# Kernel optimization log

Hardware: AMD Instinct MI355X
Metric: run time of the kernel (lower is better)

## Reference

```python
import jax, jax.numpy as jnp
import numpy as np
import math

B, L, DV = 8, 2048, 512
FACTOR = 5
SAMPLE_K = min(FACTOR * int(np.ceil(np.log(L))), L)  # 40
N_TOP = min(FACTOR * int(np.ceil(np.log(L))), L)     # 40


def setup_inputs() -> dict:
    key = jax.random.key(0)
    k1, k2, k3, k4, k5 = jax.random.split(key, 5)
    x = jax.random.normal(k1, (B, L, DV), dtype=jnp.float32)
    Wq = jax.random.normal(k2, (DV, DV), dtype=jnp.float32) * (1.0 / math.sqrt(DV))
    Wk = jax.random.normal(k3, (DV, DV), dtype=jnp.float32) * (1.0 / math.sqrt(DV))
    Wv = jax.random.normal(k4, (DV, DV), dtype=jnp.float32) * (1.0 / math.sqrt(DV))
    index_sample = jax.random.randint(k5, (L, SAMPLE_K), 0, L, dtype=jnp.int32)
    return {"x": x, "Wq": Wq, "Wk": Wk, "Wv": Wv, "index_sample": index_sample}


def reference(x, Wq, Wk, Wv, index_sample):
    # Projections (torch Linear, no bias): y = x @ W.T
    Q = x @ Wq.T  # [B, L, D]
    K = x @ Wk.T  # [B, L, D]
    V = x @ Wv.T  # [B, L, D]
    b, L_Q, D = Q.shape
    L_K = K.shape[1]

    # _prob_QK: sample keys per query, score sparsity measure M
    K_sample = K[:, index_sample, :]                       # [B, L_Q, sample_k, D]
    QK_sample = jnp.einsum('bld,blsd->bls', Q, K_sample)   # [B, L_Q, sample_k]
    M = QK_sample.max(axis=-1) - QK_sample.sum(axis=-1) / L_K  # [B, L_Q]
    _, M_top = jax.lax.top_k(M, N_TOP)                     # [B, n_top]

    Q_reduce = jnp.take_along_axis(Q, M_top[:, :, None], axis=1)  # [B, n_top, D]
    scores = jnp.einsum('bud,bkd->buk', Q_reduce, K)       # [B, n_top, L_K]
    scores = scores * (1.0 / math.sqrt(D))

    # mask_flag=False -> initial context is mean of V broadcast over queries
    attn = jax.nn.softmax(scores, axis=-1)
    context = jnp.broadcast_to(V.mean(axis=1, keepdims=True), (b, L_Q, D))
    upd = attn @ V                                         # [B, n_top, D]
    context = context.at[jnp.arange(b)[:, None], M_top].set(upd)
    return context
```

## Files before the change

### kernel.cpp

```cpp
#include <hip/hip_runtime.h>
#include <hip/hip_bf16.h>
#include <math.h>

#define BATCH 8
#define LSEQ 2048
#define DIM 512
#define SK 40
#define NTOP 40

typedef __attribute__((ext_vector_type(8))) short bf16x8;
typedef __attribute__((ext_vector_type(4))) float f32x4;

__device__ inline void split1(float f, ushort& h, ushort& l) {
    __hip_bfloat16 bh = __float2bfloat16(f);
    float r = f - __bfloat162float(bh);
    __hip_bfloat16 bl = __float2bfloat16(r);
    h = *reinterpret_cast<ushort*>(&bh);
    l = *reinterpret_cast<ushort*>(&bl);
}

__global__ __launch_bounds__(256) void convert_all(
    const float* __restrict__ x,
    const float* __restrict__ w0, const float* __restrict__ w1, const float* __restrict__ w2,
    ushort* __restrict__ xh, ushort* __restrict__ xl,
    ushort* __restrict__ wh, ushort* __restrict__ wl)
{
    const int bx = blockIdx.x;
    const float* src;
    ushort *dh, *dl;
    int i;
    if (bx < 8192) {
        i = (bx * 256 + (int)threadIdx.x) * 4;
        src = x; dh = xh; dl = xl;
    } else {
        const int j = bx - 8192;
        const int z = j >> 8;
        src = (z == 0) ? w0 : (z == 1) ? w1 : w2;
        dh = wh + (size_t)z * DIM * DIM;
        dl = wl + (size_t)z * DIM * DIM;
        i = ((j & 255) * 256 + (int)threadIdx.x) * 4;
    }
    float4 v = *reinterpret_cast<const float4*>(src + i);
    ushort4 h, l;
    split1(v.x, h.x, l.x); split1(v.y, h.y, l.y);
    split1(v.z, h.z, l.z); split1(v.w, h.w, l.w);
    *reinterpret_cast<ushort4*>(dh + i) = h;
    *reinterpret_cast<ushort4*>(dl + i) = l;
}

__device__ inline void load_lds16(const void* g, void* l) {
    __builtin_amdgcn_global_load_lds(
        (const __attribute__((address_space(1))) void*)g,
        (__attribute__((address_space(3))) void*)l, 16, 0, 0);
}

__global__ __launch_bounds__(256) void gemm_mfma(
    const ushort* __restrict__ xh, const ushort* __restrict__ xl,
    const ushort* __restrict__ whAll, const ushort* __restrict__ wlAll,
    float* __restrict__ Q, float* __restrict__ K, float* __restrict__ V)
{
    const ushort* Wh = whAll + (size_t)blockIdx.z * DIM * DIM;
    const ushort* Wl = wlAll + (size_t)blockIdx.z * DIM * DIM;
    float* C = (blockIdx.z == 0) ? Q : (blockIdx.z == 1) ? K : V;

    __shared__ ushort Ah[128 * 32], Al[128 * 32], Bh[128 * 32], Bl[128 * 32];

    const int tid  = threadIdx.x;
    const int lane = tid & 63;
    const int w    = tid >> 6;
    const int row0 = blockIdx.x * 128;
    const int col0 = blockIdx.y * 128;
    const int wr = w >> 1, wc = w & 1;

    const int rA  = w * 16 + (lane >> 2);
    const int sh_ = (lane & 3) ^ ((rA >> 1) & 3);
    const size_t aoff = (size_t)(row0 + rA) * DIM + sh_ * 8;
    const size_t boff = (size_t)(col0 + rA) * DIM + sh_ * 8;

    f32x4 acc[4][4];
    #pragma unroll
    for (int i = 0; i < 4; ++i)
        #pragma unroll
        for (int j = 0; j < 4; ++j)
            acc[i][j] = (f32x4){0.f, 0.f, 0.f, 0.f};

    const int rbA = wr * 64 + (lane & 15);
    const int rbB = wc * 64 + (lane & 15);
    const int kh  = lane >> 4;

    for (int k0 = 0; k0 < DIM; k0 += 32) {
        load_lds16(xh + aoff + k0,            &Ah[w * 512]);
        load_lds16(xh + aoff + 64 * DIM + k0, &Ah[2048 + w * 512]);
        load_lds16(xl + aoff + k0,            &Al[w * 512]);
        load_lds16(xl + aoff + 64 * DIM + k0, &Al[2048 + w * 512]);
        load_lds16(Wh + boff + k0,            &Bh[w * 512]);
        load_lds16(Wh + boff + 64 * DIM + k0, &Bh[2048 + w * 512]);
        load_lds16(Wl + boff + k0,            &Bl[w * 512]);
        load_lds16(Wl + boff + 64 * DIM + k0, &Bl[2048 + w * 512]);
        __syncthreads();

        bf16x8 fah[4], fal[4], fbh[4], fbl[4];
        #pragma unroll
        for (int mf = 0; mf < 4; ++mf) {
            const int r = rbA + mf * 16;
            const int off = r * 32 + (kh ^ ((r >> 1) & 3)) * 8;
            fah[mf] = *reinterpret_cast<const bf16x8*>(&Ah[off]);
            fal[mf] = *reinterpret_cast<const bf16x8*>(&Al[off]);
        }
        #pragma unroll
        for (int nf = 0; nf < 4; ++nf) {
            const int r = rbB + nf * 16;
            const int off = r * 32 + (kh ^ ((r >> 1) & 3)) * 8;
            fbh[nf] = *reinterpret_cast<const bf16x8*>(&Bh[off]);
            fbl[nf] = *reinterpret_cast<const bf16x8*>(&Bl[off]);
        }
        #pragma unroll
        for (int mf = 0; mf < 4; ++mf)
            #pragma unroll
            for (int nf = 0; nf < 4; ++nf) {
                acc[mf][nf] = __builtin_amdgcn_mfma_f32_16x16x32_bf16(fah[mf], fbh[nf], acc[mf][nf], 0, 0, 0);
                acc[mf][nf] = __builtin_amdgcn_mfma_f32_16x16x32_bf16(fal[mf], fbh[nf], acc[mf][nf], 0, 0, 0);
                acc[mf][nf] = __builtin_amdgcn_mfma_f32_16x16x32_bf16(fah[mf], fbl[nf], acc[mf][nf], 0, 0, 0);
            }
        __syncthreads();
    }

    #pragma unroll
    for (int mf = 0; mf < 4; ++mf)
        #pragma unroll
        for (int nf = 0; nf < 4; ++nf) {
            float* cp = C + (size_t)(row0 + wr * 64 + mf * 16 + (lane >> 4) * 4) * DIM
                          + col0 + wc * 64 + nf * 16 + (lane & 15);
            #pragma unroll
            for (int j = 0; j < 4; ++j)
                cp[(size_t)j * DIM] = acc[mf][nf][j];
        }
}

#define BM 64
#define BN 64
#define BKD 32
__global__ __launch_bounds__(256) void gemm_qkv(
    const float* __restrict__ x,
    const float* __restrict__ Wq, const float* __restrict__ Wk, const float* __restrict__ Wv,
    float* __restrict__ Q, float* __restrict__ K, float* __restrict__ V)
{
    const float* W;
    float* C;
    if (blockIdx.z == 0)      { W = Wq; C = Q; }
    else if (blockIdx.z == 1) { W = Wk; C = K; }
    else                      { W = Wv; C = V; }

    __shared__ float As[BKD][BM];
    __shared__ float Bs[BKD][BN];

    const int tid  = threadIdx.x;
    const int row0 = blockIdx.x * BM;
    const int col0 = blockIdx.y * BN;
    const int ty   = tid >> 4;
    const int tx   = tid & 15;
    const int lrow = tid >> 3;
    const int lkq  = tid & 7;

    float acc[4][4] = {};
    for (int k0 = 0; k0 < DIM; k0 += BKD) {
        #pragma unroll
        for (int h = 0; h < 2; ++h) {
            const int arow = lrow + h * 32;
            float4 va = *reinterpret_cast<const float4*>(&x[(size_t)(row0 + arow) * DIM + k0 + lkq * 4]);
            As[lkq * 4 + 0][arow] = va.x; As[lkq * 4 + 1][arow] = va.y;
            As[lkq * 4 + 2][arow] = va.z; As[lkq * 4 + 3][arow] = va.w;
            float4 vb = *reinterpret_cast<const float4*>(&W[(size_t)(col0 + arow) * DIM + k0 + lkq * 4]);
            Bs[lkq * 4 + 0][arow] = vb.x; Bs[lkq * 4 + 1][arow] = vb.y;
            Bs[lkq * 4 + 2][arow] = vb.z; Bs[lkq * 4 + 3][arow] = vb.w;
        }
        __syncthreads();
        #pragma unroll
        for (int kk = 0; kk < BKD; ++kk) {
            float4 a4 = *reinterpret_cast<const float4*>(&As[kk][ty * 4]);
            float4 b4 = *reinterpret_cast<const float4*>(&Bs[kk][tx * 4]);
            float af[4] = {a4.x, a4.y, a4.z, a4.w};
            float bf[4] = {b4.x, b4.y, b4.z, b4.w};
            #pragma unroll
            for (int i = 0; i < 4; ++i)
                #pragma unroll
                for (int j = 0; j < 4; ++j)
                    acc[i][j] += af[i] * bf[j];
        }
        __syncthreads();
    }
    #pragma unroll
    for (int i = 0; i < 4; ++i) {
        float4 o = make_float4(acc[i][0], acc[i][1], acc[i][2], acc[i][3]);
        *reinterpret_cast<float4*>(&C[(size_t)(row0 + ty * 4 + i) * DIM + col0 + tx * 4]) = o;
    }
}

__global__ __launch_bounds__(512) void m_and_vp(
    const float* __restrict__ Q, const float* __restrict__ K,
    const float* __restrict__ V, const int* __restrict__ smp,
    float* __restrict__ M, float* __restrict__ P)
{
    const int bid = blockIdx.x;
    if (bid < 2048) {
        const int wv   = threadIdx.x >> 6;
        const int lane = threadIdx.x & 63;
        const int b    = bid & 7;
        const int l    = (bid >> 3) * 8 + wv;

        const float* qr = Q + ((size_t)b * LSEQ + l) * DIM;
        float4 q0 = *reinterpret_cast<const float4*>(&qr[lane * 8]);
        float4 q1 = *reinterpret_cast<const float4*>(&qr[lane * 8 + 4]);

        const int* sp = smp + l * SK;
        const float* Kb = K + (size_t)b * LSEQ * DIM;

        float mx = -1e30f, sm = 0.0f;
        for (int s = 0; s < SK; s += 8) {
            int4 i0 = *reinterpret_cast<const int4*>(sp + s);
            int4 i1 = *reinterpret_cast<const int4*>(sp + s + 4);
            const int id[8] = {i0.x, i0.y, i0.z, i0.w, i1.x, i1.y, i1.z, i1.w};
            float p[8];
            #pragma unroll
            for (int j = 0; j < 8; ++j) {
                const float* r = Kb + (size_t)id[j] * DIM + lane * 8;
                float4 u0 = *reinterpret_cast<const float4*>(r);
                float4 u1 = *reinterpret_cast<const float4*>(r + 4);
                p[j] = q0.x*u0.x + q0.y*u0.y + q0.z*u0.z + q0.w*u0.w
                     + q1.x*u1.x + q1.y*u1.y + q1.z*u1.z + q1.w*u1.w;
            }
            #pragma unroll
            for (int o = 32; o; o >>= 1) {
                #pragma unroll
                for (int j = 0; j < 8; ++j) p[j] += __shfl_xor(p[j], o, 64);
            }
            #pragma unroll
            for (int j = 0; j < 8; ++j) { mx = fmaxf(mx, p[j]); sm += p[j]; }
        }
        if (lane == 0) M[(size_t)b * LSEQ + l] = mx - sm * (1.0f / LSEQ);
    } else {
        const int j = bid - 2048;
        const int b = j & 7, c = j >> 3;
        const int d = threadIdx.x;
        const float* vp = V + ((size_t)b * LSEQ + c * 128) * DIM + d;
        float s = 0.0f;
        for (int r = 0; r < 128; ++r) s += vp[(size_t)r * DIM];
        P[(size_t)(b * 16 + c) * DIM + d] = s;
    }
}

__global__ __launch_bounds__(512) void topk_vr(
    const float* __restrict__ M, const float* __restrict__ P,
    int* __restrict__ topidx, float* __restrict__ vmean)
{
    __shared__ float vals[LSEQ];
    __shared__ float wvv[8];
    __shared__ int   wii[8];

    if (blockIdx.x < 8) {
        const int b = blockIdx.x;
        const int tid  = threadIdx.x;
        const int lane = tid & 63;
        const int wave = tid >> 6;

        #pragma unroll
        for (int q = 0; q < 4; ++q) vals[tid + q * 512] = M[b * LSEQ + tid + q * 512];
        __syncthreads();

        for (int t = 0; t < NTOP; ++t) {
            float bv = -1e30f;
            int   bi = 0x7fffffff;
            #pragma unroll
            for (int q = 0; q < 4; ++q) {
                const int ii = tid + q * 512;
                const float v = vals[ii];
                if (v > bv) { bv = v; bi = ii; }
            }
            #pragma unroll
            for (int o = 32; o; o >>= 1) {
                float ov = __shfl_xor(bv, o, 64);
                int   oi = __shfl_xor(bi, o, 64);
                if (ov > bv || (ov == bv && oi < bi)) { bv = ov; bi = oi; }
            }
            if (lane == 0) { wvv[wave] = bv; wii[wave] = bi; }
            __syncthreads();
            if (wave == 0) {
                float fv = (lane < 8) ? wvv[lane] : -1e30f;
                int   fi = (lane < 8) ? wii[lane] : 0x7fffffff;
                #pragma unroll
                for (int o = 4; o; o >>= 1) {
                    float ov = __shfl_xor(fv, o, 64);
                    int   oi = __shfl_xor(fi, o, 64);
                    if (ov > fv || (ov == fv && oi < fi)) { fv = ov; fi = oi; }
                }
                if (lane == 0) {
                    topidx[b * NTOP + t] = fi;
                    vals[fi] = -1e30f;
                }
            }
            __syncthreads();
        }
    } else {
        const int b = blockIdx.x - 8;
        const int d = threadIdx.x;
        float s = 0.0f;
        #pragma unroll
        for (int c = 0; c < 16; ++c) s += P[(size_t)(b * 16 + c) * DIM + d];
        vmean[b * DIM + d] = s * (1.0f / LSEQ);
    }
}

__global__ __launch_bounds__(256) void fill_out(
    const float4* __restrict__ vmean4, float4* __restrict__ out4)
{
    const int f = blockIdx.x * 256 + threadIdx.x;
    const int d4 = f & 127;
    const int b  = f >> 18;
    out4[f] = vmean4[b * 128 + d4];
}

__global__ __launch_bounds__(256) void scores_kernel(
    const float* __restrict__ Q, const float* __restrict__ K,
    const int* __restrict__ topidx, float* __restrict__ S)
{
    const int b  = blockIdx.x & 7;
    const int lc = blockIdx.x >> 3;
    __shared__ float Qs[40 * 132];
    __shared__ float Ks[64 * 132];
    __shared__ int tix[NTOP];
    const int tid = threadIdx.x;
    const int lt  = tid & 31;
    const int ug  = tid >> 5;
    float acc[2][5] = {};

    if (tid < NTOP) tix[tid] = topidx[b * NTOP + tid];
    __syncthreads();

    for (int d0 = 0; d0 < DIM; d0 += 128) {
        for (int j = tid; j < 1280; j += 256) {
            const int u = j >> 5, d4 = j & 31;
            *reinterpret_cast<float4*>(&Qs[u * 132 + d4 * 4]) =
                *reinterpret_cast<const float4*>(&Q[((size_t)b * LSEQ + tix[u]) * DIM + d0 + d4 * 4]);
        }
        for (int j = tid; j < 2048; j += 256) {
            const int l = j >> 5, d4 = j & 31;
            *reinterpret_cast<float4*>(&Ks[l * 132 + d4 * 4]) =
                *reinterpret_cast<const float4*>(&K[((size_t)b * LSEQ + lc * 64 + l) * DIM + d0 + d4 * 4]);
        }
        __syncthreads();
        for (int d4 = 0; d4 < 32; ++d4) {
            float4 ka = *reinterpret_cast<const float4*>(&Ks[lt * 132 + d4 * 4]);
            float4 kb = *reinterpret_cast<const float4*>(&Ks[(lt + 32) * 132 + d4 * 4]);
            #pragma unroll
            for (int i = 0; i < 5; ++i) {
                float4 q = *reinterpret_cast<const float4*>(&Qs[(ug + i * 8) * 132 + d4 * 4]);
                acc[0][i] += q.x * ka.x + q.y * ka.y + q.z * ka.z + q.w * ka.w;
                acc[1][i] += q.x * kb.x + q.y * kb.y + q.z * kb.z + q.w * kb.w;
            }
        }
        __syncthreads();
    }
    const float scale = 0.044194173824159216f;
    #pragma unroll
    for (int i = 0; i < 5; ++i) {
        const int u = ug + i * 8;
        S[((size_t)(b * NTOP + u)) * LSEQ + lc * 64 + lt]      = acc[0][i] * scale;
        S[((size_t)(b * NTOP + u)) * LSEQ + lc * 64 + lt + 32] = acc[1][i] * scale;
    }
}

__global__ __launch_bounds__(256) void softmax_kernel(
    const float* __restrict__ S, float* __restrict__ Pt)
{
    const int row = blockIdx.x;
    const int b = row / NTOP, u = row % NTOP;
    __shared__ float red[4];
    const int tid  = threadIdx.x;
    const int lane = tid & 63;
    const int wave = tid >> 6;
    const float* sr = S + (size_t)row * LSEQ;

    float v[8];
    float mx = -1e30f;
    #pragma unroll
    for (int j = 0; j < 8; ++j) { v[j] = sr[tid + j * 256]; mx = fmaxf(mx, v[j]); }
    #pragma unroll
    for (int o = 32; o; o >>= 1) mx = fmaxf(mx, __shfl_xor(mx, o, 64));
    if (lane == 0) red[wave] = mx;
    __syncthreads();
    mx = fmaxf(fmaxf(red[0], red[1]), fmaxf(red[2], red[3]));
    __syncthreads();

    float s = 0.0f;
    #pragma unroll
    for (int j = 0; j < 8; ++j) { v[j] = __expf(v[j] - mx); s += v[j]; }
    #pragma unroll
    for (int o = 32; o; o >>= 1) s += __shfl_xor(s, o, 64);
    if (lane == 0) red[wave] = s;
    __syncthreads();
    const float rec = 1.0f / (red[0] + red[1] + red[2] + red[3]);

    #pragma unroll
    for (int j = 0; j < 8; ++j)
        Pt[((size_t)b * LSEQ + tid + j * 256) * NTOP + u] = v[j] * rec;
}

__global__ __launch_bounds__(512) void pv_partial(
    const float* __restrict__ Pt, const float* __restrict__ V, float* __restrict__ Ppart)
{
    const int b  = blockIdx.x & 7;
    const int lc = blockIdx.x >> 3;
    const int d  = threadIdx.x;
    float part[NTOP] = {};
    for (int l = 0; l < 128; ++l) {
        const float v = V[((size_t)b * LSEQ + lc * 128 + l) * DIM + d];
        const float* ps = Pt + ((size_t)b * LSEQ + lc * 128 + l) * NTOP;
        #pragma unroll
        for (int u = 0; u < NTOP; ++u) part[u] = fmaf(ps[u], v, part[u]);
    }
    #pragma unroll
    for (int u = 0; u < NTOP; ++u)
        Ppart[(((size_t)(b * 16 + lc)) * NTOP + u) * DIM + d] = part[u];
}

__global__ __launch_bounds__(512) void pv_reduce(
    const float* __restrict__ Ppart, const int* __restrict__ topidx, float* __restrict__ out)
{
    const int row = blockIdx.x;
    const int b = row / NTOP, u = row % NTOP;
    const int d = threadIdx.x;
    float s = 0.0f;
    #pragma unroll
    for (int lc = 0; lc < 16; ++lc)
        s += Ppart[(((size_t)(b * 16 + lc)) * NTOP + u) * DIM + d];
    out[((size_t)b * LSEQ + topidx[row]) * DIM + d] = s;
}

__global__ __launch_bounds__(256) void att_kernel(
    const float* __restrict__ Q, const float* __restrict__ K, const float* __restrict__ V,
    const int* __restrict__ topidx, float* __restrict__ out)
{
    const int b = blockIdx.x / NTOP;
    const int u = blockIdx.x % NTOP;
    const int l0 = topidx[b * NTOP + u];

    __shared__ float p[LSEQ];
    __shared__ float redm[4];
    __shared__ float reds[4];

    const int tid  = threadIdx.x;
    const int lane = tid & 63;
    const int wave = tid >> 6;

    const float* qr = Q + ((size_t)b * LSEQ + l0) * DIM;
    float4 q0 = *reinterpret_cast<const float4*>(&qr[lane * 8]);
    float4 q1 = *reinterpret_cast<const float4*>(&qr[lane * 8 + 4]);
    const float scale = 0.044194173824159216f;

    for (int it = 0; it < 512; ++it) {
        const int l = wave * 512 + it;
        const float* kr = K + ((size_t)b * LSEQ + l) * DIM;
        float4 k0 = *reinterpret_cast<const float4*>(&kr[lane * 8]);
        float4 k1 = *reinterpret_cast<const float4*>(&kr[lane * 8 + 4]);
        float d = q0.x * k0.x + q0.y * k0.y + q0.z * k0.z + q0.w * k0.w
                + q1.x * k1.x + q1.y * k1.y + q1.z * k1.z + q1.w * k1.w;
        #pragma unroll
        for (int o = 32; o; o >>= 1) d += __shfl_xor(d, o, 64);
        if (lane == 0) p[l] = d * scale;
    }
    __syncthreads();

    float mx = -1e30f;
    for (int i = tid; i < LSEQ; i += 256) mx = fmaxf(mx, p[i]);
    #pragma unroll
    for (int o = 32; o; o >>= 1) mx = fmaxf(mx, __shfl_xor(mx, o, 64));
    if (lane == 0) redm[wave] = mx;
    __syncthreads();
    mx = fmaxf(fmaxf(redm[0], redm[1]), fmaxf(redm[2], redm[3]));

    float s = 0.0f;
    for (int i = tid; i < LSEQ; i += 256) {
        float e = __expf(p[i] - mx);
        s += e;
        p[i] = e;
    }
    #pragma unroll
    for (int o = 32; o; o >>= 1) s += __shfl_xor(s, o, 64);
    if (lane == 0) reds[wave] = s;
    __syncthreads();
    const float rec = 1.0f / (reds[0] + reds[1] + reds[2] + reds[3]);

    float s0 = 0.0f, s1 = 0.0f;
    const float* vp = V + (size_t)b * LSEQ * DIM;
    for (int l = 0; l < LSEQ; ++l) {
        const float w = p[l];
        s0 += w * vp[(size_t)l * DIM + tid];
        s1 += w * vp[(size_t)l * DIM + tid + 256];
    }
    float* orow = out + ((size_t)b * LSEQ + l0) * DIM;
    orow[tid]       = s0 * rec;
    orow[tid + 256] = s1 * rec;
}

extern "C" void kernel_launch(void* const* d_in, const int* in_sizes, int n_in,
                              void* d_out, int out_size, void* d_ws, size_t ws_size,
                              hipStream_t stream)
{
    const float* x   = (const float*)d_in[0];
    const float* Wq  = (const float*)d_in[1];
    const float* Wk  = (const float*)d_in[2];
    const float* Wv  = (const float*)d_in[3];
    const int*   smp = (const int*)d_in[4];
    float* out = (float*)d_out;

    const size_t NQKV = (size_t)BATCH * LSEQ * DIM;
    float* ws = (float*)d_ws;

    float* Q     = ws;
    float* K     = Q + NQKV;
    float* V     = K + NQKV;
    float* Mb    = V + NQKV;
    float* vmP   = Mb + BATCH * LSEQ;
    float* vmean = vmP + BATCH * 16 * DIM;
    float* S     = vmean + BATCH * DIM;
    float* Pt    = S + (size_t)BATCH * NTOP * LSEQ;
    float* Qsel  = Pt + (size_t)BATCH * NTOP * LSEQ;
    float* Ppart = Qsel + (size_t)BATCH * NTOP * DIM;
    int*   topidx = (int*)(Ppart + (size_t)BATCH * 16 * NTOP * DIM);
    ushort* xh = (ushort*)(topidx + BATCH * NTOP);
    ushort* xl = xh + NQKV;
    ushort* wh = xl + NQKV;
    ushort* wl = wh + (size_t)3 * DIM * DIM;
    const size_t need_fast = (size_t)((char*)(wl + (size_t)3 * DIM * DIM) - (char*)d_ws);
    const size_t need_mid  = (size_t)((char*)(topidx + BATCH * NTOP) - (char*)d_ws);

    const bool fast = ws_size >= need_fast;
    const bool mid  = ws_size >= need_mid;

    if (mid) {
        if (fast) {
            convert_all<<<8960, 256, 0, stream>>>(x, Wq, Wk, Wv, xh, xl, wh, wl);
            gemm_mfma<<<dim3(BATCH * LSEQ / 128, DIM / 128, 3), 256, 0, stream>>>(
                xh, xl, wh, wl, Q, K, V);
        } else {
            gemm_qkv<<<dim3(BATCH * LSEQ / BM, DIM / BN, 3), 256, 0, stream>>>(
                x, Wq, Wk, Wv, Q, K, V);
        }
        m_and_vp<<<2176, 512, 0, stream>>>(Q, K, V, smp, Mb, vmP);
        topk_vr<<<16, 512, 0, stream>>>(Mb, vmP, topidx, vmean);
        fill_out<<<(BATCH * LSEQ * DIM / 4) / 256, 256, 0, stream>>>(
            (const float4*)vmean, (float4*)out);
        scores_kernel<<<256, 256, 0, stream>>>(Q, K, topidx, S);
        softmax_kernel<<<BATCH * NTOP, 256, 0, stream>>>(S, Pt);
        pv_partial<<<128, 512, 0, stream>>>(Pt, V, Ppart);
        pv_reduce<<<BATCH * NTOP, 512, 0, stream>>>(Ppart, topidx, out);
    } else {
        float* Qf = ws;
        float* Kf = Qf + NQKV;
        float* Vf = Kf + NQKV;
        float* Mf = Vf + NQKV;
        int*   ti = (int*)(Mf + (size_t)BATCH * LSEQ);
        float* Pf = (float*)(ti + BATCH * NTOP);
        float* vm = Pf + (size_t)BATCH * 16 * DIM;

        gemm_qkv<<<dim3(BATCH * LSEQ / BM, DIM / BN, 3), 256, 0, stream>>>(
            x, Wq, Wk, Wv, Qf, Kf, Vf);
        m_and_vp<<<2176, 512, 0, stream>>>(Qf, Kf, Vf, smp, Mf, Pf);
        topk_vr<<<16, 512, 0, stream>>>(Mf, Pf, ti, vm);
        fill_out<<<(BATCH * LSEQ * DIM / 4) / 256, 256, 0, stream>>>(
            (const float4*)vm, (float4*)out);
        att_kernel<<<BATCH * NTOP, 256, 0, stream>>>(Qf, Kf, Vf, ti, out);
    }
}
```

Baseline: 306.6 us.

## Score sparsity with fp16 K copy, refine top-k candidates in fp32

The QKV GEMM epilogue now also writes an fp16 copy of K, and the sampled-key sparsity scores read this half-width copy to cut gather traffic. Top-k is replaced by a radix-style threshold search that keeps 48-128 candidates, recomputes their scores exactly in fp32, and selects the final 40 within one wave. The PV partial kernel is also unrolled over four rows with float4 loads of the probabilities. This adds extra fp16 stores in the GEMM and a serial threshold search, and it risks picking different indices if fp16 error pushes a true top-40 query outside the candidate window.

```diff
diff --git a/kernel.cpp b/kernel.cpp
--- a/kernel.cpp
+++ b/kernel.cpp
@@ -1,5 +1,6 @@
 #include <hip/hip_runtime.h>
 #include <hip/hip_bf16.h>
+#include <hip/hip_fp16.h>
 #include <math.h>
 
 #define BATCH 8
@@ -57,11 +58,13 @@
 __global__ __launch_bounds__(256) void gemm_mfma(
     const ushort* __restrict__ xh, const ushort* __restrict__ xl,
     const ushort* __restrict__ whAll, const ushort* __restrict__ wlAll,
-    float* __restrict__ Q, float* __restrict__ K, float* __restrict__ V)
+    float* __restrict__ Q, float* __restrict__ K, float* __restrict__ V,
+    ushort* __restrict__ Khalf)
 {
     const ushort* Wh = whAll + (size_t)blockIdx.z * DIM * DIM;
     const ushort* Wl = wlAll + (size_t)blockIdx.z * DIM * DIM;
     float* C = (blockIdx.z == 0) ? Q : (blockIdx.z == 1) ? K : V;
+    const bool wk = (Khalf != nullptr) && (blockIdx.z == 1);
 
     __shared__ ushort Ah[128 * 32], Al[128 * 32], Bh[128 * 32], Bl[128 * 32];
 
@@ -129,11 +132,17 @@
     for (int mf = 0; mf < 4; ++mf)
         #pragma unroll
         for (int nf = 0; nf < 4; ++nf) {
-            float* cp = C + (size_t)(row0 + wr * 64 + mf * 16 + (lane >> 4) * 4) * DIM
-                          + col0 + wc * 64 + nf * 16 + (lane & 15);
-            #pragma unroll
-            for (int j = 0; j < 4; ++j)
+            const size_t rbase = (size_t)(row0 + wr * 64 + mf * 16 + (lane >> 4) * 4);
+            const int    cidx  = col0 + wc * 64 + nf * 16 + (lane & 15);
+            float* cp = C + rbase * DIM + cidx;
+            #pragma unroll
+            for (int j = 0; j < 4; ++j) {
                 cp[(size_t)j * DIM] = acc[mf][nf][j];
+                if (wk) {
+                    __half h = __float2half(acc[mf][nf][j]);
+                    Khalf[(rbase + j) * DIM + cidx] = *reinterpret_cast<ushort*>(&h);
+                }
+            }
         }
 }
 
@@ -198,6 +207,7 @@
 
 __global__ __launch_bounds__(512) void m_and_vp(
     const float* __restrict__ Q, const float* __restrict__ K,
+    const ushort* __restrict__ Khalf,
     const float* __restrict__ V, const int* __restrict__ smp,
     float* __restrict__ M, float* __restrict__ P)
 {
@@ -211,31 +221,58 @@
         const float* qr = Q + ((size_t)b * LSEQ + l) * DIM;
         float4 q0 = *reinterpret_cast<const float4*>(&qr[lane * 8]);
         float4 q1 = *reinterpret_cast<const float4*>(&qr[lane * 8 + 4]);
+        const float qf[8] = {q0.x, q0.y, q0.z, q0.w, q1.x, q1.y, q1.z, q1.w};
 
         const int* sp = smp + l * SK;
-        const float* Kb = K + (size_t)b * LSEQ * DIM;
-
         float mx = -1e30f, sm = 0.0f;
-        for (int s = 0; s < SK; s += 8) {
-            int4 i0 = *reinterpret_cast<const int4*>(sp + s);
-            int4 i1 = *reinterpret_cast<const int4*>(sp + s + 4);
-            const int id[8] = {i0.x, i0.y, i0.z, i0.w, i1.x, i1.y, i1.z, i1.w};
-            float p[8];
-            #pragma unroll
-            for (int j = 0; j < 8; ++j) {
-                const float* r = Kb + (size_t)id[j] * DIM + lane * 8;
-                float4 u0 = *reinterpret_cast<const float4*>(r);
-                float4 u1 = *reinterpret_cast<const float4*>(r + 4);
-                p[j] = q0.x*u0.x + q0.y*u0.y + q0.z*u0.z + q0.w*u0.w
-                     + q1.x*u1.x + q1.y*u1.y + q1.z*u1.z + q1.w*u1.w;
-            }
-            #pragma unroll
-            for (int o = 32; o; o >>= 1) {
+
+        if (Khalf) {
+            const ushort* Kb = Khalf + (size_t)b * LSEQ * DIM;
+            for (int s = 0; s < SK; s += 8) {
+                int4 i0 = *reinterpret_cast<const int4*>(sp + s);
+                int4 i1 = *reinterpret_cast<const int4*>(sp + s + 4);
+                const int id[8] = {i0.x, i0.y, i0.z, i0.w, i1.x, i1.y, i1.z, i1.w};
+                float p[8];
                 #pragma unroll
-                for (int j = 0; j < 8; ++j) p[j] += __shfl_xor(p[j], o, 64);
-            }
-            #pragma unroll
-            for (int j = 0; j < 8; ++j) { mx = fmaxf(mx, p[j]); sm += p[j]; }
+                for (int j = 0; j < 8; ++j) {
+                    float4 hv = *reinterpret_cast<const float4*>(Kb + (size_t)id[j] * DIM + lane * 8);
+                    const __half* h = reinterpret_cast<const __half*>(&hv);
+                    float d = 0.0f;
+                    #pragma unroll
+                    for (int e = 0; e < 8; ++e) d = fmaf(qf[e], __half2float(h[e]), d);
+                    p[j] = d;
+                }
+                #pragma unroll
+                for (int o = 32; o; o >>= 1) {
+                    #pragma unroll
+                    for (int j = 0; j < 8; ++j) p[j] += __shfl_xor(p[j], o, 64);
+                }
+                #pragma unroll
+                for (int j = 0; j < 8; ++j) { mx = fmaxf(mx, p[j]); sm += p[j]; }
+            }
+        } else {
+            const float* Kb = K + (size_t)b * LSEQ * DIM;
+            for (int s = 0; s < SK; s += 8) {
+                int4 i0 = *reinterpret_cast<const int4*>(sp + s);
+                int4 i1 = *reinterpret_cast<const int4*>(sp + s + 4);
+                const int id[8] = {i0.x, i0.y, i0.z, i0.w, i1.x, i1.y, i1.z, i1.w};
+                float p[8];
+                #pragma unroll
+                for (int j = 0; j < 8; ++j) {
+                    const float* r = Kb + (size_t)id[j] * DIM + lane * 8;
+                    float4 u0 = *reinterpret_cast<const float4*>(r);
+                    float4 u1 = *reinterpret_cast<const float4*>(r + 4);
+                    p[j] = q0.x*u0.x + q0.y*u0.y + q0.z*u0.z + q0.w*u0.w
+                         + q1.x*u1.x + q1.y*u1.y + q1.z*u1.z + q1.w*u1.w;
+                }
+                #pragma unroll
+                for (int o = 32; o; o >>= 1) {
+                    #pragma unroll
+                    for (int j = 0; j < 8; ++j) p[j] += __shfl_xor(p[j], o, 64);
+                }
+                #pragma unroll
+                for (int j = 0; j < 8; ++j) { mx = fmaxf(mx, p[j]); sm += p[j]; }
+            }
         }
         if (lane == 0) M[(size_t)b * LSEQ + l] = mx - sm * (1.0f / LSEQ);
     } else {
@@ -249,64 +286,139 @@
     }
 }
 
-__global__ __launch_bounds__(512) void topk_vr(
-    const float* __restrict__ M, const float* __restrict__ P,
+__device__ inline unsigned int fkey(float f) {
+    unsigned int b = __float_as_uint(f);
+    return b ^ ((b & 0x80000000u) ? 0xFFFFFFFFu : 0x80000000u);
+}
+
+__global__ __launch_bounds__(1024) void topk_refine(
+    const float* __restrict__ M, const float* __restrict__ Q,
+    const float* __restrict__ K, const int* __restrict__ smp,
+    const float* __restrict__ P,
     int* __restrict__ topidx, float* __restrict__ vmean)
 {
-    __shared__ float vals[LSEQ];
-    __shared__ float wvv[8];
-    __shared__ int   wii[8];
-
-    if (blockIdx.x < 8) {
-        const int b = blockIdx.x;
-        const int tid  = threadIdx.x;
-        const int lane = tid & 63;
-        const int wave = tid >> 6;
-
-        #pragma unroll
-        for (int q = 0; q < 4; ++q) vals[tid + q * 512] = M[b * LSEQ + tid + q * 512];
-        __syncthreads();
-
+    if (blockIdx.x >= 8) {
+        const int b = blockIdx.x - 8;
+        const int d = threadIdx.x;
+        if (d < DIM) {
+            float s = 0.0f;
+            #pragma unroll
+            for (int c = 0; c < 16; ++c) s += P[(size_t)(b * 16 + c) * DIM + d];
+            vmean[b * DIM + d] = s * (1.0f / LSEQ);
+        }
+        return;
+    }
+
+    const int b    = blockIdx.x;
+    const int tid  = threadIdx.x;
+    const int lane = tid & 63;
+    const int wave = tid >> 6;
+
+    __shared__ int   cand[1024];
+    __shared__ float Mex[1024];
+    __shared__ int   scnt[16];
+    __shared__ int   sh_tot;
+    __shared__ int   sh_ccnt;
+
+    const unsigned int k0 = fkey(M[(size_t)b * LSEQ + tid]);
+    const unsigned int k1 = fkey(M[(size_t)b * LSEQ + tid + 1024]);
+    Mex[tid] = -1e30f;
+    if (tid == 0) sh_ccnt = 0;
+    __syncthreads();
+
+    unsigned int lo = 0u, hi = 0xFFFFFFFFu, T = 0u, Tbest = 0u;
+    int found = 0;
+    for (int it = 0; it < 32; ++it) {
+        unsigned int mid = lo + ((hi - lo) >> 1);
+        int c = (k0 > mid ? 1 : 0) + (k1 > mid ? 1 : 0);
+        #pragma unroll
+        for (int o = 32; o; o >>= 1) c += __shfl_xor(c, o, 64);
+        if (lane == 0) scnt[wave] = c;
+        __syncthreads();
+        if (tid == 0) {
+            int t2 = 0;
+            #pragma unroll
+            for (int ww = 0; ww < 16; ++ww) t2 += scnt[ww];
+            sh_tot = t2;
+        }
+        __syncthreads();
+        const int tot = sh_tot;
+        __syncthreads();
+        if (tot >= 48 && tot <= 128) { T = mid; found = 1; break; }
+        if (tot >= 48 && mid > Tbest) Tbest = mid;
+        if (tot > 128) { if (mid == 0xFFFFFFFFu) break; lo = mid + 1; }
+        else           { if (mid == 0u) break; hi = mid - 1; }
+        if (lo > hi) break;
+    }
+    if (!found) T = Tbest;
+
+    if (k0 > T) { int p = atomicAdd(&sh_ccnt, 1); if (p < 1024) cand[p] = tid; }
+    if (k1 > T) { int p = atomicAdd(&sh_ccnt, 1); if (p < 1024) cand[p] = tid + 1024; }
+    __syncthreads();
+    const int n = min(sh_ccnt, 1024);
+
+    for (int j = wave; j < n; j += 16) {
+        const int l = cand[j];
+        const float* qr = Q + ((size_t)b * LSEQ + l) * DIM;
+        float4 q0 = *reinterpret_cast<const float4*>(&qr[lane * 8]);
+        float4 q1 = *reinterpret_cast<const float4*>(&qr[lane * 8 + 4]);
+        const int* sp = smp + l * SK;
+        const float* Kb = K + (size_t)b * LSEQ * DIM;
+        float mx = -1e30f, sm = 0.0f;
+        for (int s = 0; s < SK; s += 8) {
+            int4 i0 = *reinterpret_cast<const int4*>(sp + s);
+            int4 i1 = *reinterpret_cast<const int4*>(sp + s + 4);
+            const int id[8] = {i0.x, i0.y, i0.z, i0.w, i1.x, i1.y, i1.z, i1.w};
+            float p[8];
+            #pragma unroll
+            for (int jj = 0; jj < 8; ++jj) {
+                const float* r = Kb + (size_t)id[jj] * DIM + lane * 8;
+                float4 u0 = *reinterpret_cast<const float4*>(r);
+                float4 u1 = *reinterpret_cast<const float4*>(r + 4);
+                p[jj] = q0.x*u0.x + q0.y*u0.y + q0.z*u0.z + q0.w*u0.w
+                      + q1.x*u1.x + q1.y*u1.y + q1.z*u1.z + q1.w*u1.w;
+            }
+            #pragma unroll
+            for (int o = 32; o; o >>= 1) {
+                #pragma unroll
+                for (int jj = 0; jj < 8; ++jj) p[jj] += __shfl_xor(p[jj], o, 64);
+            }
+            #pragma unroll
+            for (int jj = 0; jj < 8; ++jj) { mx = fmaxf(mx, p[jj]); sm += p[jj]; }
+        }
+        if (lane == 0) Mex[j] = mx - sm * (1.0f / LSEQ);
+    }
+    __syncthreads();
+
+    if (wave == 0) {
+        float lv[16];
+        int   cl[16];
+        #pragma unroll
+        for (int kk = 0; kk < 16; ++kk) {
+            const int j = lane + kk * 64;
+            lv[kk] = Mex[j];
+            cl[kk] = cand[j];
+        }
         for (int t = 0; t < NTOP; ++t) {
-            float bv = -1e30f;
-            int   bi = 0x7fffffff;
-            #pragma unroll
-            for (int q = 0; q < 4; ++q) {
-                const int ii = tid + q * 512;
-                const float v = vals[ii];
-                if (v > bv) { bv = v; bi = ii; }
-            }
+            float bv = -1e30f; int bl = 0x7fffffff; int bk = -1;
+            #pragma unroll
+            for (int kk = 0; kk < 16; ++kk) {
+                if (lv[kk] > bv || (lv[kk] == bv && cl[kk] < bl)) {
+                    bv = lv[kk]; bl = cl[kk]; bk = kk;
+                }
+            }
+            int blane = lane;
             #pragma unroll
             for (int o = 32; o; o >>= 1) {
                 float ov = __shfl_xor(bv, o, 64);
-                int   oi = __shfl_xor(bi, o, 64);
-                if (ov > bv || (ov == bv && oi < bi)) { bv = ov; bi = oi; }
-            }
-            if (lane == 0) { wvv[wave] = bv; wii[wave] = bi; }
-            __syncthreads();
-            if (wave == 0) {
-                float fv = (lane < 8) ? wvv[lane] : -1e30f;
-                int   fi = (lane < 8) ? wii[lane] : 0x7fffffff;
-                #pragma unroll
-                for (int o = 4; o; o >>= 1) {
-                    float ov = __shfl_xor(fv, o, 64);
-                    int   oi = __shfl_xor(fi, o, 64);
-                    if (ov > fv || (ov == fv && oi < fi)) { fv = ov; fi = oi; }
-                }
-                if (lane == 0) {
-                    topidx[b * NTOP + t] = fi;
-                    vals[fi] = -1e30f;
-                }
-            }
-            __syncthreads();
-        }
-    } else {
-        const int b = blockIdx.x - 8;
-        const int d = threadIdx.x;
-        float s = 0.0f;
-        #pragma unroll
-        for (int c = 0; c < 16; ++c) s += P[(size_t)(b * 16 + c) * DIM + d];
-        vmean[b * DIM + d] = s * (1.0f / LSEQ);
+                int   ol = __shfl_xor(bl, o, 64);
+                int   oln = __shfl_xor(blane, o, 64);
+                int   obk = __shfl_xor(bk, o, 64);
+                if (ov > bv || (ov == bv && ol < bl)) { bv = ov; bl = ol; blane = oln; bk = obk; }
+            }
+            if (lane == 0) topidx[b * NTOP + t] = bl;
+            if (lane == blane) lv[bk] = -1e30f;
+        }
     }
 }
 
@@ -412,11 +524,24 @@
     const int lc = blockIdx.x >> 3;
     const int d  = threadIdx.x;
     float part[NTOP] = {};
-    for (int l = 0; l < 128; ++l) {
-        const float v = V[((size_t)b * LSEQ + lc * 128 + l) * DIM + d];
-        const float* ps = Pt + ((size_t)b * LSEQ + lc * 128 + l) * NTOP;
-        #pragma unroll
-        for (int u = 0; u < NTOP; ++u) part[u] = fmaf(ps[u], v, part[u]);
+    for (int lg = 0; lg < 32; ++lg) {
+        const int l = lc * 128 + lg * 4;
+        const float v0 = V[((size_t)b * LSEQ + l + 0) * DIM + d];
+        const float v1 = V[((size_t)b * LSEQ + l + 1) * DIM + d];
+        const float v2 = V[((size_t)b * LSEQ + l + 2) * DIM + d];
+        const float v3 = V[((size_t)b * LSEQ + l + 3) * DIM + d];
+        const float4* p0 = reinterpret_cast<const float4*>(Pt + ((size_t)b * LSEQ + l + 0) * NTOP);
+        const float4* p1 = reinterpret_cast<const float4*>(Pt + ((size_t)b * LSEQ + l + 1) * NTOP);
+        const float4* p2 = reinterpret_cast<const float4*>(Pt + ((size_t)b * LSEQ + l + 2) * NTOP);
+        const float4* p3 = reinterpret_cast<const float4*>(Pt + ((size_t)b * LSEQ + l + 3) * NTOP);
+        #pragma unroll
+        for (int u4 = 0; u4 < 10; ++u4) {
+            float4 a = p0[u4], bb = p1[u4], c = p2[u4], dd = p3[u4];
+            part[u4*4+0] = fmaf(a.x, v0, fmaf(bb.x, v1, fmaf(c.x, v2, fmaf(dd.x, v3, part[u4*4+0]))));
+            part[u4*4+1] = fmaf(a.y, v0, fmaf(bb.y, v1, fmaf(c.y, v2, fmaf(dd.y, v3, part[u4*4+1]))));
+            part[u4*4+2] = fmaf(a.z, v0, fmaf(bb.z, v1, fmaf(c.z, v2, fmaf(dd.z, v3, part[u4*4+2]))));
+            part[u4*4+3] = fmaf(a.w, v0, fmaf(bb.w, v1, fmaf(c.w, v2, fmaf(dd.w, v3, part[u4*4+3]))));
+        }
     }
     #pragma unroll
     for (int u = 0; u < NTOP; ++u)
@@ -531,23 +656,28 @@
     ushort* xl = xh + NQKV;
     ushort* wh = xl + NQKV;
     ushort* wl = wh + (size_t)3 * DIM * DIM;
-    const size_t need_fast = (size_t)((char*)(wl + (size_t)3 * DIM * DIM) - (char*)d_ws);
-    const size_t need_mid  = (size_t)((char*)(topidx + BATCH * NTOP) - (char*)d_ws);
-
-    const bool fast = ws_size >= need_fast;
-    const bool mid  = ws_size >= need_mid;
+    ushort* Khalf = wl + (size_t)3 * DIM * DIM;
+    const size_t need_fast2 = (size_t)((char*)(Khalf + NQKV) - (char*)d_ws);
+    const size_t need_fast  = (size_t)((char*)Khalf - (char*)d_ws);
+    const size_t need_mid   = (size_t)((char*)(topidx + BATCH * NTOP) - (char*)d_ws);
+
+    const bool fast2 = ws_size >= need_fast2;
+    const bool fast  = ws_size >= need_fast;
+    const bool mid   = ws_size >= need_mid;
 
     if (mid) {
+        ushort* kh = fast2 ? Khalf : nullptr;
         if (fast) {
             convert_all<<<8960, 256, 0, stream>>>(x, Wq, Wk, Wv, xh, xl, wh, wl);
             gemm_mfma<<<dim3(BATCH * LSEQ / 128, DIM / 128, 3), 256, 0, stream>>>(
-                xh, xl, wh, wl, Q, K, V);
+                xh, xl, wh, wl, Q, K, V, kh);
         } else {
             gemm_qkv<<<dim3(BATCH * LSEQ / BM, DIM / BN, 3), 256, 0, stream>>>(
                 x, Wq, Wk, Wv, Q, K, V);
-        }
-        m_and_vp<<<2176, 512, 0, stream>>>(Q, K, V, smp, Mb, vmP);
-        topk_vr<<<16, 512, 0, stream>>>(Mb, vmP, topidx, vmean);
+            kh = nullptr;
+        }
+        m_and_vp<<<2176, 512, 0, stream>>>(Q, K, kh, V, smp, Mb, vmP);
+        topk_refine<<<16, 1024, 0, stream>>>(Mb, Q, K, smp, vmP, topidx, vmean);
         fill_out<<<(BATCH * LSEQ * DIM / 4) / 256, 256, 0, stream>>>(
             (const float4*)vmean, (float4*)out);
         scores_kernel<<<256, 256, 0, stream>>>(Q, K, topidx, S);
@@ -565,8 +695,8 @@
 
         gemm_qkv<<<dim3(BATCH * LSEQ / BM, DIM / BN, 3), 256, 0, stream>>>(
             x, Wq, Wk, Wv, Qf, Kf, Vf);
-        m_and_vp<<<2176, 512, 0, stream>>>(Qf, Kf, Vf, smp, Mf, Pf);
-        topk_vr<<<16, 512, 0, stream>>>(Mf, Pf, ti, vm);
+        m_and_vp<<<2176, 512, 0, stream>>>(Qf, Kf, nullptr, Vf, smp, Mf, Pf);
+        topk_refine<<<16, 1024, 0, stream>>>(Mf, Qf, Kf, smp, Pf, ti, vm);
         fill_out<<<(BATCH * LSEQ * DIM / 4) / 256, 256, 0, stream>>>(
             (const float4*)vm, (float4*)out);
         att_kernel<<<BATCH * NTOP, 256, 0, stream>>>(Qf, Kf, Vf, ti, out);
```

Result: slower. 398.1 us (+29.8%).
